# Optimization experiments

Measured on AMD Instinct MI355X. Metric: run time of the kernel, lower is better.

## Reference

```python
import jax, jax.numpy as jnp
import numpy as np

B, S, D = 64, 1024, 512  # batch, seq, input_size == hidden_size


def setup_inputs() -> dict:
    key = jax.random.key(0)
    ks = jax.random.split(key, 5)
    scale = 1.0 / np.sqrt(D)
    x = jax.random.normal(ks[0], (B, S, D), dtype=jnp.float32)
    W_ih = jax.random.uniform(ks[1], (D, D), jnp.float32, -scale, scale)
    b_ih = jax.random.uniform(ks[2], (D,), jnp.float32, -scale, scale)
    W_hh = jax.random.uniform(ks[3], (D, D), jnp.float32, -scale, scale)
    b_hh = jax.random.uniform(ks[4], (D,), jnp.float32, -scale, scale)
    return {"x": x, "W_ih": W_ih, "b_ih": b_ih, "W_hh": W_hh, "b_hh": b_hh}


def reference(x, W_ih, b_ih, W_hh, b_hh):
    # Precompute the input projection for all timesteps (same math, batched GEMM)
    xt_all = jnp.einsum('bsd,hd->bsh', x, W_ih) + b_ih  # [B,S,H]
    prev0 = jnp.zeros((x.shape[0], W_hh.shape[0]), dtype=x.dtype)

    def step(prev, xt):
        ht = jnp.tanh(xt + prev @ W_hh.T + b_hh)
        return ht, ht

    # scan over time: xt_all transposed to [S,B,H]
    last, hs = jax.lax.scan(step, prev0, jnp.swapaxes(xt_all, 0, 1))
    output = jnp.swapaxes(hs, 0, 1)  # [B,S,H]
    return output, last
```

## Files before the change

kernel.cpp:

```cpp
#include <hip/hip_runtime.h>

#define BB 64
#define SS 1024
#define HH 512

typedef short short8 __attribute__((ext_vector_type(8)));
typedef float f32x4 __attribute__((ext_vector_type(4)));
typedef _Float16 h2 __attribute__((ext_vector_type(2)));

__device__ inline unsigned short f2bf(float f) {
  unsigned int u = __builtin_bit_cast(unsigned int, f);
  u += 0x7fffu + ((u >> 16) & 1u);
  return (unsigned short)(u >> 16);
}

__device__ inline unsigned int pack_h2(float a, float b) {
  unsigned short ua = __builtin_bit_cast(unsigned short, (_Float16)a);
  unsigned short ub = __builtin_bit_cast(unsigned short, (_Float16)b);
  return (unsigned int)ua | ((unsigned int)ub << 16);
}

__device__ inline float dot2a(unsigned int w, unsigned int h, float acc) {
#if __has_builtin(__builtin_amdgcn_fdot2)
  return __builtin_amdgcn_fdot2(__builtin_bit_cast(h2, w),
                                __builtin_bit_cast(h2, h), acc, false);
#else
  h2 a = __builtin_bit_cast(h2, w);
  h2 b = __builtin_bit_cast(h2, h);
  return acc + (float)a[0] * (float)b[0] + (float)a[1] * (float)b[1];
#endif
}

__global__ __launch_bounds__(256) void xt_gemm(
    const float* __restrict__ x, const float* __restrict__ Wih,
    const float* __restrict__ bih, float* __restrict__ out) {
  __shared__ unsigned short As[64][56];
  __shared__ unsigned short Bs[64][56];

  const int bn = blockIdx.x;
  const int bm = blockIdx.y;
  const int t = threadIdx.x;
  const int wave = t >> 6, lane = t & 63;
  const int wm = wave >> 1, wn = wave & 1;
  const int m_base = bm * 64, n_base = bn * 64;
  const int sr = t >> 2;
  const int sc = (t & 3) * 8;

  f32x4 acc[2][2] = {};

  for (int k0 = 0; k0 < 512; k0 += 32) {
    __syncthreads();
    {
      const float* p = x + (size_t)(m_base + sr) * 512 + k0 + sc;
      float4 v0 = *(const float4*)p;
      float4 v1 = *(const float4*)(p + 4);
      short8 sa;
      sa[0] = (short)f2bf(v0.x); sa[1] = (short)f2bf(v0.y);
      sa[2] = (short)f2bf(v0.z); sa[3] = (short)f2bf(v0.w);
      sa[4] = (short)f2bf(v1.x); sa[5] = (short)f2bf(v1.y);
      sa[6] = (short)f2bf(v1.z); sa[7] = (short)f2bf(v1.w);
      *(short8*)&As[sr][sc] = sa;

      const float* q = Wih + (size_t)(n_base + sr) * 512 + k0 + sc;
      float4 w0 = *(const float4*)q;
      float4 w1 = *(const float4*)(q + 4);
      short8 sb;
      sb[0] = (short)f2bf(w0.x); sb[1] = (short)f2bf(w0.y);
      sb[2] = (short)f2bf(w0.z); sb[3] = (short)f2bf(w0.w);
      sb[4] = (short)f2bf(w1.x); sb[5] = (short)f2bf(w1.y);
      sb[6] = (short)f2bf(w1.z); sb[7] = (short)f2bf(w1.w);
      *(short8*)&Bs[sr][sc] = sb;
    }
    __syncthreads();

    const int kq = (lane >> 4) * 8;
    short8 a0 = *(const short8*)&As[wm * 32 + (lane & 15)][kq];
    short8 a1 = *(const short8*)&As[wm * 32 + 16 + (lane & 15)][kq];
    short8 b0 = *(const short8*)&Bs[wn * 32 + (lane & 15)][kq];
    short8 b1 = *(const short8*)&Bs[wn * 32 + 16 + (lane & 15)][kq];
    acc[0][0] = __builtin_amdgcn_mfma_f32_16x16x32_bf16(a0, b0, acc[0][0], 0, 0, 0);
    acc[0][1] = __builtin_amdgcn_mfma_f32_16x16x32_bf16(a0, b1, acc[0][1], 0, 0, 0);
    acc[1][0] = __builtin_amdgcn_mfma_f32_16x16x32_bf16(a1, b0, acc[1][0], 0, 0, 0);
    acc[1][1] = __builtin_amdgcn_mfma_f32_16x16x32_bf16(a1, b1, acc[1][1], 0, 0, 0);
  }

#pragma unroll
  for (int ni = 0; ni < 2; ++ni) {
    const int gcol = n_base + wn * 32 + ni * 16 + (lane & 15);
    const float bv = bih[gcol];
#pragma unroll
    for (int mi = 0; mi < 2; ++mi) {
#pragma unroll
      for (int j = 0; j < 4; ++j) {
        const int grow = m_base + wm * 32 + mi * 16 + (lane >> 4) * 4 + j;
        out[(size_t)grow * 512 + gcol] = acc[mi][ni][j] + bv;
      }
    }
  }
}

__global__
__attribute__((amdgpu_flat_work_group_size(512, 512)))
__attribute__((amdgpu_waves_per_eu(2, 2)))
void rnn_scan(
    const float* __restrict__ Whh, const float* __restrict__ bhh,
    float* __restrict__ out, float* __restrict__ last) {
  __shared__ uint4 wlds[16 * 512];
  __shared__ float part[8 * 512];
  __shared__ unsigned short hbuf[512];

  const int b = blockIdx.x;
  const int t = threadIdx.x;
  const int kg = t >> 6;
  const int hg = t & 63;
  const int k0 = kg * 64;

  unsigned int wreg[6][32];
#pragma unroll
  for (int i = 0; i < 6; ++i) {
    const float* wr = Whh + (size_t)(hg + 64 * i) * 512 + k0;
#pragma unroll
    for (int c4 = 0; c4 < 16; ++c4) {
      float4 f = ((const float4*)wr)[c4];
      wreg[i][c4 * 2]     = pack_h2(f.x, f.y);
      wreg[i][c4 * 2 + 1] = pack_h2(f.z, f.w);
    }
  }
#pragma unroll
  for (int i = 0; i < 6; ++i) {
#pragma unroll
    for (int d = 0; d < 32; ++d) {
      asm volatile("" : "+v"(wreg[i][d]));
    }
  }

#pragma unroll
  for (int i = 6; i < 8; ++i) {
    const float* wr = Whh + (size_t)(hg + 64 * i) * 512 + k0;
#pragma unroll
    for (int c = 0; c < 8; ++c) {
      float4 f0 = ((const float4*)wr)[c * 2];
      float4 f1 = ((const float4*)wr)[c * 2 + 1];
      uint4 v;
      v.x = pack_h2(f0.x, f0.y); v.y = pack_h2(f0.z, f0.w);
      v.z = pack_h2(f1.x, f1.y); v.w = pack_h2(f1.z, f1.w);
      wlds[((i - 6) * 8 + c) * 512 + t] = v;
    }
  }
  if (t < 256) ((unsigned int*)hbuf)[t] = 0;

  float* xt_row = out + (size_t)b * SS * HH;
  float xt_cur = xt_row[t];
  const float bh = bhh[t];
  const uint4* h4 = (const uint4*)hbuf + kg * 8;
  __syncthreads();

  for (int step = 0; step < SS; ++step) {
    float xt_next = 0.f;
    if (step + 1 < SS) xt_next = xt_row[(size_t)(step + 1) * HH + t];

    float a[8] = {0.f, 0.f, 0.f, 0.f, 0.f, 0.f, 0.f, 0.f};
#pragma unroll
    for (int c = 0; c < 8; ++c) {
      uint4 hv = h4[c];
      uint4 w6 = wlds[c * 512 + t];
      uint4 w7 = wlds[(8 + c) * 512 + t];
      a[0] = dot2a(wreg[0][4 * c + 0], hv.x, a[0]);
      a[0] = dot2a(wreg[0][4 * c + 1], hv.y, a[0]);
      a[0] = dot2a(wreg[0][4 * c + 2], hv.z, a[0]);
      a[0] = dot2a(wreg[0][4 * c + 3], hv.w, a[0]);
      a[1] = dot2a(wreg[1][4 * c + 0], hv.x, a[1]);
      a[1] = dot2a(wreg[1][4 * c + 1], hv.y, a[1]);
      a[1] = dot2a(wreg[1][4 * c + 2], hv.z, a[1]);
      a[1] = dot2a(wreg[1][4 * c + 3], hv.w, a[1]);
      a[2] = dot2a(wreg[2][4 * c + 0], hv.x, a[2]);
      a[2] = dot2a(wreg[2][4 * c + 1], hv.y, a[2]);
      a[2] = dot2a(wreg[2][4 * c + 2], hv.z, a[2]);
      a[2] = dot2a(wreg[2][4 * c + 3], hv.w, a[2]);
      a[3] = dot2a(wreg[3][4 * c + 0], hv.x, a[3]);
      a[3] = dot2a(wreg[3][4 * c + 1], hv.y, a[3]);
      a[3] = dot2a(wreg[3][4 * c + 2], hv.z, a[3]);
      a[3] = dot2a(wreg[3][4 * c + 3], hv.w, a[3]);
      a[4] = dot2a(wreg[4][4 * c + 0], hv.x, a[4]);
      a[4] = dot2a(wreg[4][4 * c + 1], hv.y, a[4]);
      a[4] = dot2a(wreg[4][4 * c + 2], hv.z, a[4]);
      a[4] = dot2a(wreg[4][4 * c + 3], hv.w, a[4]);
      a[5] = dot2a(wreg[5][4 * c + 0], hv.x, a[5]);
      a[5] = dot2a(wreg[5][4 * c + 1], hv.y, a[5]);
      a[5] = dot2a(wreg[5][4 * c + 2], hv.z, a[5]);
      a[5] = dot2a(wreg[5][4 * c + 3], hv.w, a[5]);
      a[6] = dot2a(w6.x, hv.x, a[6]);
      a[6] = dot2a(w6.y, hv.y, a[6]);
      a[6] = dot2a(w6.z, hv.z, a[6]);
      a[6] = dot2a(w6.w, hv.w, a[6]);
      a[7] = dot2a(w7.x, hv.x, a[7]);
      a[7] = dot2a(w7.y, hv.y, a[7]);
      a[7] = dot2a(w7.z, hv.z, a[7]);
      a[7] = dot2a(w7.w, hv.w, a[7]);
    }
#pragma unroll
    for (int i = 0; i < 8; ++i) part[kg * 512 + hg + 64 * i] = a[i];
    __syncthreads();

    float y = xt_cur + bh;
#pragma unroll
    for (int g = 0; g < 8; ++g) y += part[g * 512 + t];
    float ht = tanhf(y);
    xt_row[(size_t)step * HH + t] = ht;
    hbuf[t] = __builtin_bit_cast(unsigned short, (_Float16)ht);
    xt_cur = xt_next;
    __syncthreads();
  }

  last[(size_t)b * HH + t] = xt_row[(size_t)(SS - 1) * HH + t];
}

extern "C" void kernel_launch(void* const* d_in, const int* in_sizes, int n_in,
                              void* d_out, int out_size, void* d_ws, size_t ws_size,
                              hipStream_t stream) {
  (void)in_sizes; (void)n_in; (void)d_ws; (void)ws_size; (void)out_size;
  const float* x   = (const float*)d_in[0];
  const float* Wih = (const float*)d_in[1];
  const float* bih = (const float*)d_in[2];
  const float* Whh = (const float*)d_in[3];
  const float* bhh = (const float*)d_in[4];
  float* out  = (float*)d_out;
  float* last = out + (size_t)BB * SS * HH;

  xt_gemm<<<dim3(8, 1024), 256, 0, stream>>>(x, Wih, bih, out);

  rnn_scan<<<64, 512, 0, stream>>>(Whh, bhh, out, last);
}
```

Before: 1.619 ms.

## Stream most recurrent weight rows from global workspace instead of registers

Drops the waves_per_eu constraint and keeps only one of eight W_hh row-groups in registers and two in LDS. The remaining five are pre-packed to fp16 by a new kernel into the workspace and streamed from global memory (L2) every timestep with double-buffered loads. This frees register pressure and may improve scheduling, but it adds roughly 320KB of global/L2 weight traffic per block per step on the serial critical path.

```diff
diff --git a/kernel.cpp b/kernel.cpp
--- a/kernel.cpp
+++ b/kernel.cpp
@@ -29,6 +29,22 @@
   h2 b = __builtin_bit_cast(h2, h);
   return acc + (float)a[0] * (float)b[0] + (float)a[1] * (float)b[1];
 #endif
+}
+
+__global__ __launch_bounds__(512) void pack_ws(
+    const float* __restrict__ Whh, uint4* __restrict__ ws4) {
+  const int L = blockIdx.x;
+  const int t = threadIdx.x;
+  const int kg = t >> 6, hg = t & 63;
+  const int row = hg + 64 * (3 + (L >> 3));
+  const int k0 = kg * 64 + (L & 7) * 8;
+  const float* p = Whh + (size_t)row * HH + k0;
+  float4 f0 = ((const float4*)p)[0];
+  float4 f1 = ((const float4*)p)[1];
+  uint4 v;
+  v.x = pack_h2(f0.x, f0.y); v.y = pack_h2(f0.z, f0.w);
+  v.z = pack_h2(f1.x, f1.y); v.w = pack_h2(f1.z, f1.w);
+  ws4[(size_t)L * 512 + t] = v;
 }
 
 __global__ __launch_bounds__(256) void xt_gemm(
@@ -101,10 +117,9 @@
 
 __global__
 __attribute__((amdgpu_flat_work_group_size(512, 512)))
-__attribute__((amdgpu_waves_per_eu(2, 2)))
-void rnn_scan(
-    const float* __restrict__ Whh, const float* __restrict__ bhh,
-    float* __restrict__ out, float* __restrict__ last) {
+void rnn_scan(const float* __restrict__ Whh, const float* __restrict__ bhh,
+              float* __restrict__ out, float* __restrict__ last,
+              const uint4* __restrict__ ws4) {
   __shared__ uint4 wlds[16 * 512];
   __shared__ float part[8 * 512];
   __shared__ unsigned short hbuf[512];
@@ -115,27 +130,18 @@
   const int hg = t & 63;
   const int k0 = kg * 64;
 
-  unsigned int wreg[6][32];
-#pragma unroll
-  for (int i = 0; i < 6; ++i) {
-    const float* wr = Whh + (size_t)(hg + 64 * i) * 512 + k0;
+  unsigned int wreg[32];
+  {
+    const float* wr = Whh + (size_t)hg * 512 + k0;
 #pragma unroll
     for (int c4 = 0; c4 < 16; ++c4) {
       float4 f = ((const float4*)wr)[c4];
-      wreg[i][c4 * 2]     = pack_h2(f.x, f.y);
-      wreg[i][c4 * 2 + 1] = pack_h2(f.z, f.w);
-    }
-  }
-#pragma unroll
-  for (int i = 0; i < 6; ++i) {
-#pragma unroll
-    for (int d = 0; d < 32; ++d) {
-      asm volatile("" : "+v"(wreg[i][d]));
-    }
-  }
-
-#pragma unroll
-  for (int i = 6; i < 8; ++i) {
+      wreg[c4 * 2]     = pack_h2(f.x, f.y);
+      wreg[c4 * 2 + 1] = pack_h2(f.z, f.w);
+    }
+  }
+#pragma unroll
+  for (int i = 1; i < 3; ++i) {
     const float* wr = Whh + (size_t)(hg + 64 * i) * 512 + k0;
 #pragma unroll
     for (int c = 0; c < 8; ++c) {
@@ -144,7 +150,7 @@
       uint4 v;
       v.x = pack_h2(f0.x, f0.y); v.y = pack_h2(f0.z, f0.w);
       v.z = pack_h2(f1.x, f1.y); v.w = pack_h2(f1.z, f1.w);
-      wlds[((i - 6) * 8 + c) * 512 + t] = v;
+      wlds[((i - 1) * 8 + c) * 512 + t] = v;
     }
   }
   if (t < 256) ((unsigned int*)hbuf)[t] = 0;
@@ -153,53 +159,79 @@
   float xt_cur = xt_row[t];
   const float bh = bhh[t];
   const uint4* h4 = (const uint4*)hbuf + kg * 8;
+  const uint4* wsp = ws4 + t;
   __syncthreads();
+
+#define SLOAD(v0, v1, v2, v3, Lb)        \
+  v0 = wsp[((Lb) * 4 + 0) * 512];        \
+  v1 = wsp[((Lb) * 4 + 1) * 512];        \
+  v2 = wsp[((Lb) * 4 + 2) * 512];        \
+  v3 = wsp[((Lb) * 4 + 3) * 512];
+
+#define SCONS(v0, v1, v2, v3, ai, j)                              \
+  acc_[ai] = dot2a(v0.x, hr[(j) * 4 + 0].x, acc_[ai]);            \
+  acc_[ai] = dot2a(v0.y, hr[(j) * 4 + 0].y, acc_[ai]);            \
+  acc_[ai] = dot2a(v0.z, hr[(j) * 4 + 0].z, acc_[ai]);            \
+  acc_[ai] = dot2a(v0.w, hr[(j) * 4 + 0].w, acc_[ai]);            \
+  acc_[ai] = dot2a(v1.x, hr[(j) * 4 + 1].x, acc_[ai]);            \
+  acc_[ai] = dot2a(v1.y, hr[(j) * 4 + 1].y, acc_[ai]);            \
+  acc_[ai] = dot2a(v1.z, hr[(j) * 4 + 1].z, acc_[ai]);            \
+  acc_[ai] = dot2a(v1.w, hr[(j) * 4 + 1].w, acc_[ai]);            \
+  acc_[ai] = dot2a(v2.x, hr[(j) * 4 + 2].x, acc_[ai]);            \
+  acc_[ai] = dot2a(v2.y, hr[(j) * 4 + 2].y, acc_[ai]);            \
+  acc_[ai] = dot2a(v2.z, hr[(j) * 4 + 2].z, acc_[ai]);            \
+  acc_[ai] = dot2a(v2.w, hr[(j) * 4 + 2].w, acc_[ai]);            \
+  acc_[ai] = dot2a(v3.x, hr[(j) * 4 + 3].x, acc_[ai]);            \
+  acc_[ai] = dot2a(v3.y, hr[(j) * 4 + 3].y, acc_[ai]);            \
+  acc_[ai] = dot2a(v3.z, hr[(j) * 4 + 3].z, acc_[ai]);            \
+  acc_[ai] = dot2a(v3.w, hr[(j) * 4 + 3].w, acc_[ai]);
 
   for (int step = 0; step < SS; ++step) {
     float xt_next = 0.f;
     if (step + 1 < SS) xt_next = xt_row[(size_t)(step + 1) * HH + t];
 
-    float a[8] = {0.f, 0.f, 0.f, 0.f, 0.f, 0.f, 0.f, 0.f};
+    uint4 hr[8];
+#pragma unroll
+    for (int c = 0; c < 8; ++c) hr[c] = hbuf ? h4[c] : hr[c];
+
+    uint4 A0, A1, A2, A3, B0, B1, B2, B3;
+    SLOAD(A0, A1, A2, A3, 0);
+    SLOAD(B0, B1, B2, B3, 1);
+
+    float acc_[8] = {0.f, 0.f, 0.f, 0.f, 0.f, 0.f, 0.f, 0.f};
 #pragma unroll
     for (int c = 0; c < 8; ++c) {
-      uint4 hv = h4[c];
-      uint4 w6 = wlds[c * 512 + t];
-      uint4 w7 = wlds[(8 + c) * 512 + t];
-      a[0] = dot2a(wreg[0][4 * c + 0], hv.x, a[0]);
-      a[0] = dot2a(wreg[0][4 * c + 1], hv.y, a[0]);
-      a[0] = dot2a(wreg[0][4 * c + 2], hv.z, a[0]);
-      a[0] = dot2a(wreg[0][4 * c + 3], hv.w, a[0]);
-      a[1] = dot2a(wreg[1][4 * c + 0], hv.x, a[1]);
-      a[1] = dot2a(wreg[1][4 * c + 1], hv.y, a[1]);
-      a[1] = dot2a(wreg[1][4 * c + 2], hv.z, a[1]);
-      a[1] = dot2a(wreg[1][4 * c + 3], hv.w, a[1]);
-      a[2] = dot2a(wreg[2][4 * c + 0], hv.x, a[2]);
-      a[2] = dot2a(wreg[2][4 * c + 1], hv.y, a[2]);
-      a[2] = dot2a(wreg[2][4 * c + 2], hv.z, a[2]);
-      a[2] = dot2a(wreg[2][4 * c + 3], hv.w, a[2]);
-      a[3] = dot2a(wreg[3][4 * c + 0], hv.x, a[3]);
-      a[3] = dot2a(wreg[3][4 * c + 1], hv.y, a[3]);
-      a[3] = dot2a(wreg[3][4 * c + 2], hv.z, a[3]);
-      a[3] = dot2a(wreg[3][4 * c + 3], hv.w, a[3]);
-      a[4] = dot2a(wreg[4][4 * c + 0], hv.x, a[4]);
-      a[4] = dot2a(wreg[4][4 * c + 1], hv.y, a[4]);
-      a[4] = dot2a(wreg[4][4 * c + 2], hv.z, a[4]);
-      a[4] = dot2a(wreg[4][4 * c + 3], hv.w, a[4]);
-      a[5] = dot2a(wreg[5][4 * c + 0], hv.x, a[5]);
-      a[5] = dot2a(wreg[5][4 * c + 1], hv.y, a[5]);
-      a[5] = dot2a(wreg[5][4 * c + 2], hv.z, a[5]);
-      a[5] = dot2a(wreg[5][4 * c + 3], hv.w, a[5]);
-      a[6] = dot2a(w6.x, hv.x, a[6]);
-      a[6] = dot2a(w6.y, hv.y, a[6]);
-      a[6] = dot2a(w6.z, hv.z, a[6]);
-      a[6] = dot2a(w6.w, hv.w, a[6]);
-      a[7] = dot2a(w7.x, hv.x, a[7]);
-      a[7] = dot2a(w7.y, hv.y, a[7]);
-      a[7] = dot2a(w7.z, hv.z, a[7]);
-      a[7] = dot2a(w7.w, hv.w, a[7]);
-    }
-#pragma unroll
-    for (int i = 0; i < 8; ++i) part[kg * 512 + hg + 64 * i] = a[i];
+      acc_[0] = dot2a(wreg[4 * c + 0], hr[c].x, acc_[0]);
+      acc_[0] = dot2a(wreg[4 * c + 1], hr[c].y, acc_[0]);
+      acc_[0] = dot2a(wreg[4 * c + 2], hr[c].z, acc_[0]);
+      acc_[0] = dot2a(wreg[4 * c + 3], hr[c].w, acc_[0]);
+    }
+#pragma unroll
+    for (int c = 0; c < 8; ++c) {
+      uint4 w1 = wlds[c * 512 + t];
+      uint4 w2 = wlds[(8 + c) * 512 + t];
+      acc_[1] = dot2a(w1.x, hr[c].x, acc_[1]);
+      acc_[1] = dot2a(w1.y, hr[c].y, acc_[1]);
+      acc_[1] = dot2a(w1.z, hr[c].z, acc_[1]);
+      acc_[1] = dot2a(w1.w, hr[c].w, acc_[1]);
+      acc_[2] = dot2a(w2.x, hr[c].x, acc_[2]);
+      acc_[2] = dot2a(w2.y, hr[c].y, acc_[2]);
+      acc_[2] = dot2a(w2.z, hr[c].z, acc_[2]);
+      acc_[2] = dot2a(w2.w, hr[c].w, acc_[2]);
+    }
+    SCONS(A0, A1, A2, A3, 3, 0); SLOAD(A0, A1, A2, A3, 2);
+    SCONS(B0, B1, B2, B3, 3, 1); SLOAD(B0, B1, B2, B3, 3);
+    SCONS(A0, A1, A2, A3, 4, 0); SLOAD(A0, A1, A2, A3, 4);
+    SCONS(B0, B1, B2, B3, 4, 1); SLOAD(B0, B1, B2, B3, 5);
+    SCONS(A0, A1, A2, A3, 5, 0); SLOAD(A0, A1, A2, A3, 6);
+    SCONS(B0, B1, B2, B3, 5, 1); SLOAD(B0, B1, B2, B3, 7);
+    SCONS(A0, A1, A2, A3, 6, 0); SLOAD(A0, A1, A2, A3, 8);
+    SCONS(B0, B1, B2, B3, 6, 1); SLOAD(B0, B1, B2, B3, 9);
+    SCONS(A0, A1, A2, A3, 7, 0);
+    SCONS(B0, B1, B2, B3, 7, 1);
+
+#pragma unroll
+    for (int i = 0; i < 8; ++i) part[kg * 512 + hg + 64 * i] = acc_[i];
     __syncthreads();
 
     float y = xt_cur + bh;
@@ -213,12 +245,14 @@
   }
 
   last[(size_t)b * HH + t] = xt_row[(size_t)(SS - 1) * HH + t];
+#undef SLOAD
+#undef SCONS
 }
 
 extern "C" void kernel_launch(void* const* d_in, const int* in_sizes, int n_in,
                               void* d_out, int out_size, void* d_ws, size_t ws_size,
                               hipStream_t stream) {
-  (void)in_sizes; (void)n_in; (void)d_ws; (void)ws_size; (void)out_size;
+  (void)in_sizes; (void)n_in; (void)ws_size; (void)out_size;
   const float* x   = (const float*)d_in[0];
   const float* Wih = (const float*)d_in[1];
   const float* bih = (const float*)d_in[2];
@@ -226,8 +260,11 @@
   const float* bhh = (const float*)d_in[4];
   float* out  = (float*)d_out;
   float* last = out + (size_t)BB * SS * HH;
+  uint4* ws4  = (uint4*)d_ws;
+
+  pack_ws<<<40, 512, 0, stream>>>(Whh, ws4);
 
   xt_gemm<<<dim3(8, 1024), 256, 0, stream>>>(x, Wih, bih, out);
 
-  rnn_scan<<<64, 512, 0, stream>>>(Whh, bhh, out, last);
-}
+  rnn_scan<<<64, 512, 0, stream>>>(Whh, bhh, out, last, ws4);
+}
```

Result: slower. 1.730 ms (+6.8%).
